# Kernel tuning notes

Measured on AMD Instinct MI355X. Metric: run time of the kernel, lower is better.

The kernel has to match this reference:

```python
import jax, jax.numpy as jnp
import numpy as np
import math

D = 256; H = 8; L = 6; DK = D // H

def _ln(x, g, b):
    m = jnp.mean(x, -1, keepdims=True)
    v = jnp.mean((x - m) ** 2, -1, keepdims=True)
    return (x - m) * jax.lax.rsqrt(v + 1e-5) * g + b

def setup_inputs() -> dict:
    key = jax.random.key(0)
    ks = jax.random.split(key, 16)
    B, N, F, E = 8, 768, 128, 4
    s = 0.02
    inp = {}
    inp['node_feats'] = jax.random.normal(ks[0], (B, N, F), jnp.float32)
    inp['adj'] = jax.random.randint(ks[1], (B, N, N), 0, 2, jnp.int32)
    inp['dist'] = jax.random.uniform(ks[2], (B, N, N), jnp.float32)
    inp['edge_type_oh'] = jax.random.uniform(ks[3], (B, N, N, E), jnp.float32)
    inp['node_proj_w'] = jax.random.normal(ks[4], (F, D), jnp.float32) * s
    inp['node_proj_b'] = jnp.zeros((D,), jnp.float32)
    inp['cls'] = jax.random.normal(ks[5], (1, 1, D), jnp.float32) * s
    inp['etw'] = jax.random.normal(ks[6], (E,), jnp.float32) * s
    inp['noedge_bias'] = jnp.float32(-2.0)
    inp['deg_scale'] = jnp.float32(0.2)
    inp['gamma'] = jnp.float32(0.8)
    inp['v2n'] = jnp.float32(0.1)
    inp['n2v'] = jnp.float32(0.1)
    inp['vself'] = jnp.float32(0.05)
    inp['ln1_g'] = jnp.ones((L, D), jnp.float32); inp['ln1_b'] = jnp.zeros((L, D), jnp.float32)
    inp['qw'] = jax.random.normal(ks[7], (L, D, D), jnp.float32) * s; inp['qb'] = jnp.zeros((L, D), jnp.float32)
    inp['kw'] = jax.random.normal(ks[8], (L, D, D), jnp.float32) * s; inp['kb'] = jnp.zeros((L, D), jnp.float32)
    inp['vw'] = jax.random.normal(ks[9], (L, D, D), jnp.float32) * s; inp['vb'] = jnp.zeros((L, D), jnp.float32)
    inp['ow'] = jax.random.normal(ks[10], (L, D, D), jnp.float32) * s; inp['ob'] = jnp.zeros((L, D), jnp.float32)
    inp['ln2_g'] = jnp.ones((L, D), jnp.float32); inp['ln2_b'] = jnp.zeros((L, D), jnp.float32)
    Dm = int(D * 1.0)  # mlp_ratio=1.0
    inp['fc1w'] = jax.random.normal(ks[11], (L, D, Dm), jnp.float32) * s; inp['fc1b'] = jnp.zeros((L, Dm), jnp.float32)
    inp['fc2w'] = jax.random.normal(ks[12], (L, Dm, D), jnp.float32) * s; inp['fc2b'] = jnp.zeros((L, D), jnp.float32)
    return inp

def _build_bias(adj_f, dist, edge_type_oh, etw, noedge_bias, deg_scale, gamma, v2n, n2v, vself):
    # DynamicAttnBiasBuilder: hard_mask=False, use_degree=True, vnode_spd_mode='replace', gamma != 0
    B, N, _ = adj_f.shape
    T = N + 1
    e = jnp.einsum('bije,e->bij', edge_type_oh, etw) - gamma * dist  # (B,N,N)
    e = jnp.where(adj_f > 0, e, e + noedge_bias)
    deg = adj_f.sum(-1)  # (B,N)
    deg_norm = (deg[:, :, None] + deg[:, None, :]) / (deg.max(axis=1, keepdims=True)[:, :, None] + 1e-6)
    e = e + deg_scale * deg_norm
    bias = jnp.zeros((B, T, T), jnp.float32)
    bias = bias.at[:, 1:, 1:].set(e)
    bias = bias.at[:, 0, 1:].set(v2n)   # vnode_spd_mode == 'replace'
    bias = bias.at[:, 1:, 0].set(n2v)
    bias = bias.at[:, 0, 0].set(vself)
    return bias  # (B,T,T), broadcast over heads

def _mhsa(x, bias, qw, qb, kw, kb, vw, vb, ow, ob):
    B, T, _ = x.shape
    q = (x @ qw + qb).reshape(B, T, H, DK).transpose(0, 2, 1, 3)
    k = (x @ kw + kb).reshape(B, T, H, DK).transpose(0, 2, 1, 3)
    v = (x @ vw + vb).reshape(B, T, H, DK).transpose(0, 2, 1, 3)
    scores = jnp.einsum('bhqd,bhkd->bhqk', q, k) / math.sqrt(DK)
    scores = scores + bias[:, None, :, :]
    attn = jax.nn.softmax(scores, axis=-1)
    out = jnp.einsum('bhqk,bhkd->bhqd', attn, v)
    out = out.transpose(0, 2, 1, 3).reshape(B, T, D)
    return out @ ow + ob

def _forward(node_feats, adj, dist, edge_type_oh, node_proj_w, node_proj_b, cls,
             etw, noedge_bias, deg_scale, gamma, v2n, n2v, vself,
             ln1_g, ln1_b, qw, qb, kw, kb, vw, vb, ow, ob,
             ln2_g, ln2_b, fc1w, fc1b, fc2w, fc2b):
    adj_f = adj.astype(jnp.float32)
    bias = _build_bias(adj_f, dist, edge_type_oh, etw, noedge_bias, deg_scale, gamma, v2n, n2v, vself)
    B = node_feats.shape[0]
    x = node_feats @ node_proj_w + node_proj_b  # (B,N,D)
    x = jnp.concatenate([jnp.broadcast_to(cls, (B, 1, D)), x], axis=1)  # prepend virtual node -> (B,T,D)
    for l in range(L):
        h = _mhsa(_ln(x, ln1_g[l], ln1_b[l]), bias, qw[l], qb[l], kw[l], kb[l], vw[l], vb[l], ow[l], ob[l])
        x = x + h
        m = _ln(x, ln2_g[l], ln2_b[l])
        m = jax.nn.gelu(m @ fc1w[l] + fc1b[l], approximate=False) @ fc2w[l] + fc2b[l]
        x = x + m
    return x

def reference(node_feats, adj, dist, edge_type_oh, node_proj_w, node_proj_b, cls,
              etw, noedge_bias, deg_scale, gamma, v2n, n2v, vself,
              ln1_g, ln1_b, qw, qb, kw, kb, vw, vb, ow, ob,
              ln2_g, ln2_b, fc1w, fc1b, fc2w, fc2b):
    return _forward(node_feats, adj, dist, edge_type_oh, node_proj_w, node_proj_b, cls,
                    etw, noedge_bias, deg_scale, gamma, v2n, n2v, vself,
                    ln1_g, ln1_b, qw, qb, kw, kb, vw, vb, ow, ob,
                    ln2_g, ln2_b, fc1w, fc1b, fc2w, fc2b)
```

## Files before the change

### kernel.cpp

```cpp
#include <hip/hip_runtime.h>
#include <math.h>

#define BB 8
#define NN 768
#define TT 769
#define DD 256
#define HH 8
#define DKK 32
#define FF 128
#define LL 6
#define MM 6152
#define SCALE 0.17677669529663687f
#define TP 832
#define KQP 784
#define KHS (KQP * DKK)
#define GBP 776
#define HP 264
#define WSZ 65536

typedef __attribute__((ext_vector_type(8))) short s16x8;
typedef __attribute__((ext_vector_type(8))) unsigned short u16x8;
typedef __attribute__((ext_vector_type(4))) float f32x4;

__device__ inline short f2bf(float x) {
    unsigned u = __float_as_uint(x);
    unsigned r = (u + 0x7FFFu + ((u >> 16) & 1u)) >> 16;
    return (short)r;
}
__device__ inline float bf2f(unsigned short s) {
    return __uint_as_float(((unsigned)s) << 16);
}
__device__ inline float gelu_f(float x) {
    return 0.5f * x * (1.f + erff(x * 0.70710678118654752f));
}

__global__ __launch_bounds__(256) void deg_kernel(const int* __restrict__ adj,
                                                  float* __restrict__ deg) {
    int row  = blockIdx.x * 4 + (threadIdx.x >> 6);
    int lane = threadIdx.x & 63;
    const int* p = adj + (size_t)row * NN;
    int s = 0;
#pragma unroll
    for (int i = 0; i < NN / 64; ++i) s += p[lane + 64 * i];
#pragma unroll
    for (int off = 32; off > 0; off >>= 1) s += __shfl_xor(s, off);
    if (lane == 0) deg[row] = (float)s;
}

__global__ __launch_bounds__(256) void degmax_kernel(const float* __restrict__ deg,
                                                     float* __restrict__ dmax) {
    __shared__ float red[256];
    int b = blockIdx.x, t = threadIdx.x;
    float m = 0.f;
    for (int i = t; i < NN; i += 256) m = fmaxf(m, deg[b * NN + i]);
    red[t] = m;
    __syncthreads();
    for (int s = 128; s > 0; s >>= 1) {
        if (t < s) red[t] = fmaxf(red[t], red[t + s]);
        __syncthreads();
    }
    if (t == 0) dmax[b] = red[0];
}

__global__ __launch_bounds__(256) void bias_kernel(
    const float* __restrict__ dist, const float* __restrict__ eoh,
    const int* __restrict__ adj, const float* __restrict__ deg,
    const float* __restrict__ dmax, const float* __restrict__ etw,
    const float* __restrict__ noedge, const float* __restrict__ degsc,
    const float* __restrict__ gamma, const float* __restrict__ v2n,
    const float* __restrict__ n2v, const float* __restrict__ vself,
    unsigned short* __restrict__ bias)
{
    long long idx = (long long)blockIdx.x * 256 + threadIdx.x;
    const long long total = (long long)BB * TT * GBP;
    if (idx >= total) return;
    int b  = (int)(idx / ((long long)TT * GBP));
    int r  = (int)(idx % ((long long)TT * GBP));
    int qi = r / GBP, kj = r % GBP;
    float out;
    if (kj >= TT)                out = 0.f;
    else if (qi == 0 && kj == 0) out = vself[0];
    else if (qi == 0)            out = v2n[0];
    else if (kj == 0)            out = n2v[0];
    else {
        int i = qi - 1, j = kj - 1;
        size_t e = ((size_t)b * NN + i) * NN + j;
        float4 oh = *(const float4*)(eoh + 4 * e);
        float val = oh.x * etw[0] + oh.y * etw[1] + oh.z * etw[2] + oh.w * etw[3]
                    - gamma[0] * dist[e];
        if (adj[e] == 0) val += noedge[0];
        val += degsc[0] * (deg[b * NN + i] + deg[b * NN + j]) / (dmax[b] + 1e-6f);
        out = val;
    }
    bias[idx] = (unsigned short)f2bf(out);
}

__global__ __launch_bounds__(256) void nodeproj_ln_kernel(
    const float* __restrict__ nf, const float* __restrict__ w,
    const float* __restrict__ bsv, const float* __restrict__ cls,
    const float* __restrict__ g, const float* __restrict__ bvec,
    float* __restrict__ x, short* __restrict__ xn)
{
    __shared__ float sf[FF];
    __shared__ float red[256];
    int row = blockIdx.x, t = threadIdx.x;
    int b = row / TT, tr = row % TT;
    float y;
    if (tr == 0) {
        y = cls[t];
    } else {
        if (t < FF) sf[t] = nf[((size_t)b * NN + tr - 1) * FF + t];
        __syncthreads();
        y = bsv[t];
#pragma unroll 8
        for (int kk = 0; kk < FF; ++kk) y = fmaf(sf[kk], w[kk * DD + t], y);
    }
    x[(size_t)row * DD + t] = y;
    red[t] = y;
    __syncthreads();
    for (int s = 128; s > 0; s >>= 1) { if (t < s) red[t] += red[t + s]; __syncthreads(); }
    float mean = red[0] * (1.f / DD);
    __syncthreads();
    float d = y - mean;
    red[t] = d * d;
    __syncthreads();
    for (int s = 128; s > 0; s >>= 1) { if (t < s) red[t] += red[t + s]; __syncthreads(); }
    float var = red[0] * (1.f / DD);
    xn[(size_t)row * DD + t] = f2bf(d * rsqrtf(var + 1e-5f) * g[t] + bvec[t]);
}

__global__ __launch_bounds__(256) void wtrans_kernel(
    const float* __restrict__ qw, const float* __restrict__ kw,
    const float* __restrict__ vw, const float* __restrict__ ow,
    const float* __restrict__ f1w, const float* __restrict__ f2w,
    short* __restrict__ wt2)
{
    int mi = blockIdx.x >> 4, kg = blockIdx.x & 15;
    int fam = mi / 6, l = mi % 6;
    const float* W;
    if      (fam == 0) W = qw;
    else if (fam == 1) W = kw;
    else if (fam == 2) W = vw;
    else if (fam == 3) W = ow;
    else if (fam == 4) W = f1w;
    else               W = f2w;
    W += (size_t)l * DD * DD;
    int n = threadIdx.x;
    short* out = wt2 + (size_t)mi * WSZ;
#pragma unroll
    for (int kk = 0; kk < 16; ++kk) {
        int k = kg * 16 + kk;
        float val = W[(size_t)k * DD + n];
        size_t idx = (size_t)(((n >> 4) * 8 + (k >> 5)) * 512
                   + (((k >> 3) & 3) * 16 + (n & 15)) * 8 + (k & 7));
        out[idx] = f2bf(val);
    }
}

__global__ __launch_bounds__(256) void gemm_qkv_kernel(
    const short* __restrict__ A, const short* __restrict__ wtl,
    const float* __restrict__ qb, const float* __restrict__ kb,
    const float* __restrict__ vb,
    short* __restrict__ qh, short* __restrict__ kh, short* __restrict__ vtb)
{
    int t = threadIdx.x;
    int w = t >> 6, lane = t & 63, quad = lane >> 4, m16 = lane & 15;
    int m0 = blockIdx.x * 16;
    int fam = blockIdx.y;
    const short* Wf = wtl + (size_t)fam * 6 * WSZ;
    const float* bsv = fam == 0 ? qb : (fam == 1 ? kb : vb);
    int arow = m0 + m16; if (arow >= MM) arow = MM - 1;
    const short* ap = A + (size_t)arow * DD + quad * 8;
    const short* wbase = Wf + (size_t)(w * 4) * 4096 + lane * 8;
    f32x4 acc[4] = {};
#pragma unroll
    for (int kc = 0; kc < 8; ++kc) {
        s16x8 af = *(const s16x8*)(ap + kc * 32);
#pragma unroll
        for (int nt = 0; nt < 4; ++nt) {
            s16x8 bf = *(const s16x8*)(wbase + (size_t)nt * 4096 + kc * 512);
            acc[nt] = __builtin_amdgcn_mfma_f32_16x16x32_bf16(af, bf, acc[nt], 0, 0, 0);
        }
    }
    if (fam < 2) {
        short* outp = fam == 0 ? qh : kh;
#pragma unroll
        for (int r = 0; r < 4; ++r) {
            int row = m0 + quad * 4 + r;
            if (row < MM) {
                int b = row / TT;
                int tpos = row - b * TT;
                size_t rb = ((size_t)b * HH * KQP + tpos) * DKK;
#pragma unroll
                for (int nt = 0; nt < 4; ++nt) {
                    int col = w * 64 + nt * 16 + m16;
                    float bv = bsv[col];
                    int h = col >> 5, dk = col & 31;
                    outp[rb + (size_t)h * KHS + dk] = f2bf(acc[nt][r] + bv);
                }
            }
        }
    } else {
#pragma unroll
        for (int nt = 0; nt < 4; ++nt) {
            int col = w * 64 + nt * 16 + m16;
            float bv = bsv[col];
            int h = col >> 5, dk = col & 31;
#pragma unroll
            for (int r = 0; r < 4; ++r) {
                int row = m0 + quad * 4 + r;
                if (row < MM) {
                    int b = row / TT;
                    int tpos = row - b * TT;
                    vtb[(((size_t)(b * HH + h)) * DKK + dk) * TP + tpos] =
                        f2bf(acc[nt][r] + bv);
                }
            }
        }
    }
}

__global__ __launch_bounds__(256) void attn_kernel(
    const short* __restrict__ q, const short* __restrict__ k,
    const short* __restrict__ vt, const unsigned short* __restrict__ bias,
    short* __restrict__ o)
{
    __shared__ short Pb[4][16][72];
    int t = threadIdx.x;
    int wid = t >> 6, lane = t & 63;
    int quad = lane >> 4, m16 = lane & 15;
    int bx = blockIdx.x;
    int h4 = bx / 392;
    int rem = bx - h4 * 392;
    int b = rem / 49;
    int qt = rem - b * 49;
    int h = h4 * 4 + wid;
    int q0 = qt * 16;

    size_t rb4[4];
#pragma unroll
    for (int r = 0; r < 4; ++r) {
        int qr = q0 + quad * 4 + r; if (qr >= TT) qr = TT - 1;
        rb4[r] = (size_t)(b * TT + qr) * GBP;
    }

    int qrow = q0 + m16;
    int qc = qrow < TT ? qrow : TT - 1;
    const short* qbase = q + (size_t)(b * HH + h) * KHS;
    s16x8 qa = *(const s16x8*)(qbase + (size_t)qc * DKK + quad * 8);

    const short* kbase = k + (size_t)(b * HH + h) * KHS;
    const short* vbase = vt + (((size_t)(b * HH + h)) * DKK) * TP;

    s16x8 kfA[4], kfB[4], vfA[4], vfB[4];
    unsigned short bbA[16], bbB[16];
    f32x4 sacc[4];
    f32x4 o0 = {0.f, 0.f, 0.f, 0.f};
    f32x4 o1 = {0.f, 0.f, 0.f, 0.f};
    float ls[4] = {0.f, 0.f, 0.f, 0.f};

#define LOADK_(DST, CC)                                                         \
    {                                                                           \
        _Pragma("unroll") for (int s = 0; s < 4; ++s) {                         \
            int kr = (CC) * 64 + s * 16 + m16;                                  \
            int kcl = kr < TT ? kr : TT - 1;                                    \
            DST[s] = *(const s16x8*)(kbase + (size_t)kcl * DKK + quad * 8);     \
        }                                                                       \
    }
#define LOADV_(DST, CC)                                                         \
    {                                                                           \
        int jn = (CC) * 64;                                                     \
        DST[0] = *(const s16x8*)(vbase + (size_t)m16 * TP + jn + quad * 8);     \
        DST[1] = *(const s16x8*)(vbase + (size_t)m16 * TP + jn + 32 + quad * 8);\
        DST[2] = *(const s16x8*)(vbase + (size_t)(16 + m16) * TP + jn + quad * 8);\
        DST[3] = *(const s16x8*)(vbase + (size_t)(16 + m16) * TP + jn + 32 + quad * 8);\
    }
#define LOADB_(DST, CC)                                                         \
    {                                                                           \
        _Pragma("unroll") for (int s = 0; s < 4; ++s) {                         \
            int ko = (CC) * 64 + s * 16 + m16;                                  \
            ko = ko < TT ? ko : 0;                                              \
            _Pragma("unroll") for (int r = 0; r < 4; ++r)                       \
                DST[s * 4 + r] = bias[rb4[r] + ko];                             \
        }                                                                       \
    }
#define STEP_(C, KPRE, KUSE, VUSE, VPRE, BUSE, BPRE, DOPREK, DOPREV, DOPREB, DOQK) \
    {                                                                           \
        if (DOPREK) LOADK_(KPRE, (C) + 2);                                      \
        if (DOPREV) LOADV_(VPRE, (C) + 1);                                      \
        if (DOPREB) LOADB_(BPRE, (C) + 1);                                      \
        int j0 = (C) * 64;                                                      \
        _Pragma("unroll") for (int s = 0; s < 4; ++s) {                         \
            int key = j0 + s * 16 + m16;                                        \
            int kv = key < TT;                                                  \
            _Pragma("unroll") for (int r = 0; r < 4; ++r) {                     \
                float bv = bf2f(BUSE[s * 4 + r]);                               \
                float sval = kv ? fmaf(sacc[s][r], SCALE, bv) : -1e30f;         \
                float p = __expf(sval - 8.0f);                                  \
                ls[r] += p;                                                     \
                Pb[wid][quad * 4 + r][s * 16 + m16] = f2bf(p);                  \
            }                                                                   \
        }                                                                       \
        if (DOQK) {                                                             \
            f32x4 z = {0.f, 0.f, 0.f, 0.f};                                     \
            _Pragma("unroll") for (int s = 0; s < 4; ++s)                       \
                sacc[s] = __builtin_amdgcn_mfma_f32_16x16x32_bf16(qa, KUSE[s], z, 0, 0, 0); \
        }                                                                       \
        s16x8 pa0 = *(const s16x8*)&Pb[wid][m16][quad * 8];                     \
        s16x8 pa1 = *(const s16x8*)&Pb[wid][m16][32 + quad * 8];                \
        o0 = __builtin_amdgcn_mfma_f32_16x16x32_bf16(pa0, VUSE[0], o0, 0, 0, 0);\
        o0 = __builtin_amdgcn_mfma_f32_16x16x32_bf16(pa1, VUSE[1], o0, 0, 0, 0);\
        o1 = __builtin_amdgcn_mfma_f32_16x16x32_bf16(pa0, VUSE[2], o1, 0, 0, 0);\
        o1 = __builtin_amdgcn_mfma_f32_16x16x32_bf16(pa1, VUSE[3], o1, 0, 0, 0);\
    }

    LOADK_(kfA, 0);
    LOADK_(kfB, 1);
    LOADV_(vfA, 0);
    LOADB_(bbA, 0);
    {
        f32x4 z = {0.f, 0.f, 0.f, 0.f};
#pragma unroll
        for (int s = 0; s < 4; ++s)
            sacc[s] = __builtin_amdgcn_mfma_f32_16x16x32_bf16(qa, kfA[s], z, 0, 0, 0);
    }

    for (int cc = 0; cc < 5; ++cc) {
        STEP_(2 * cc,     kfA, kfB, vfA, vfB, bbA, bbB, 1, 1, 1, 1)
        STEP_(2 * cc + 1, kfB, kfA, vfB, vfA, bbB, bbA, 1, 1, 1, 1)
    }
    STEP_(10, kfA, kfB, vfA, vfB, bbA, bbB, 1, 1, 1, 1)
    STEP_(11, kfB, kfA, vfB, vfA, bbB, bbA, 0, 1, 1, 1)
    STEP_(12, kfA, kfB, vfA, vfB, bbA, bbB, 0, 0, 0, 0)

#undef STEP_
#undef LOADB_
#undef LOADV_
#undef LOADK_

#pragma unroll
    for (int r = 0; r < 4; ++r) {
        float l = ls[r];
#pragma unroll
        for (int off = 1; off < 16; off <<= 1) l += __shfl_xor(l, off);
        int qr = q0 + quad * 4 + r;
        if (qr < TT) {
            float inv = 1.f / l;
            short* op = o + ((size_t)(b * TT + qr)) * DD + h * DKK;
            op[m16]      = f2bf(o0[r] * inv);
            op[16 + m16] = f2bf(o1[r] * inv);
        }
    }
}

__global__ __launch_bounds__(256) void gemm_oln2_kernel(
    const short* __restrict__ A, const short* __restrict__ Ws,
    const float* __restrict__ bsv, const float* __restrict__ g2,
    const float* __restrict__ b2, float* __restrict__ x, short* __restrict__ xn)
{
    __shared__ float redS[64], redQ[64];
    int t = threadIdx.x;
    int w = t >> 6, lane = t & 63, quad = lane >> 4, m16 = lane & 15;
    int m0 = blockIdx.x * 16;
    int arow = m0 + m16; if (arow >= MM) arow = MM - 1;
    const short* ap = A + (size_t)arow * DD + quad * 8;
    const short* wbase = Ws + (size_t)(w * 4) * 4096 + lane * 8;
    f32x4 acc[4] = {};
#pragma unroll
    for (int kc = 0; kc < 8; ++kc) {
        s16x8 af = *(const s16x8*)(ap + kc * 32);
#pragma unroll
        for (int nt = 0; nt < 4; ++nt) {
            s16x8 bf = *(const s16x8*)(wbase + (size_t)nt * 4096 + kc * 512);
            acc[nt] = __builtin_amdgcn_mfma_f32_16x16x32_bf16(af, bf, acc[nt], 0, 0, 0);
        }
    }
    float vv[4][4], sr[4], qr2[4];
#pragma unroll
    for (int r = 0; r < 4; ++r) { sr[r] = 0.f; qr2[r] = 0.f; }
#pragma unroll
    for (int nt = 0; nt < 4; ++nt) {
        int col = w * 64 + nt * 16 + m16;
        float bv = bsv[col];
#pragma unroll
        for (int r = 0; r < 4; ++r) {
            int row = m0 + quad * 4 + r; int rc = row < MM ? row : MM - 1;
            float v = acc[nt][r] + bv + x[(size_t)rc * DD + col];
            vv[nt][r] = v; sr[r] += v; qr2[r] += v * v;
        }
    }
#pragma unroll
    for (int r = 0; r < 4; ++r)
#pragma unroll
        for (int off = 1; off < 16; off <<= 1) {
            sr[r]  += __shfl_xor(sr[r], off);
            qr2[r] += __shfl_xor(qr2[r], off);
        }
    if (m16 == 0) {
#pragma unroll
        for (int r = 0; r < 4; ++r) {
            redS[w * 16 + quad * 4 + r] = sr[r];
            redQ[w * 16 + quad * 4 + r] = qr2[r];
        }
    }
    __syncthreads();
#pragma unroll
    for (int r = 0; r < 4; ++r) {
        int rl = quad * 4 + r;
        int row = m0 + rl;
        float fs = redS[rl] + redS[16 + rl] + redS[32 + rl] + redS[48 + rl];
        float fq = redQ[rl] + redQ[16 + rl] + redQ[32 + rl] + redQ[48 + rl];
        float mean = fs * (1.f / DD);
        float var = fq * (1.f / DD) - mean * mean;
        float inv = rsqrtf(var + 1e-5f);
        if (row < MM) {
#pragma unroll
            for (int nt = 0; nt < 4; ++nt) {
                int col = w * 64 + nt * 16 + m16;
                float v = vv[nt][r];
                x[(size_t)row * DD + col] = v;
                xn[(size_t)row * DD + col] = f2bf((v - mean) * inv * g2[col] + b2[col]);
            }
        }
    }
}

__global__ __launch_bounds__(256) void mlp_kernel(
    short* __restrict__ xn, const short* __restrict__ W1s,
    const short* __restrict__ W2s, const float* __restrict__ f1b,
    const float* __restrict__ f2b, float* __restrict__ x,
    const float* __restrict__ g1, const float* __restrict__ b1, int donext)
{
    __shared__ short hbuf[16 * HP];
    __shared__ float redS[64], redQ[64];
    int t = threadIdx.x;
    int w = t >> 6, lane = t & 63, quad = lane >> 4, m16 = lane & 15;
    int m0 = blockIdx.x * 16;
    int arow = m0 + m16; if (arow >= MM) arow = MM - 1;
    const short* ap = xn + (size_t)arow * DD + quad * 8;
    const short* w1base = W1s + (size_t)(w * 4) * 4096 + lane * 8;
    const short* w2base = W2s + (size_t)(w * 4) * 4096 + lane * 8;

    f32x4 acc[4] = {};
#pragma unroll
    for (int kc = 0; kc < 8; ++kc) {
        s16x8 af = *(const s16x8*)(ap + kc * 32);
#pragma unroll
        for (int nt = 0; nt < 4; ++nt) {
            s16x8 bf = *(const s16x8*)(w1base + (size_t)nt * 4096 + kc * 512);
            acc[nt] = __builtin_amdgcn_mfma_f32_16x16x32_bf16(af, bf, acc[nt], 0, 0, 0);
        }
    }
#pragma unroll
    for (int nt = 0; nt < 4; ++nt) {
        int col = w * 64 + nt * 16 + m16;
        float fb = f1b[col];
#pragma unroll
        for (int r = 0; r < 4; ++r)
            hbuf[(quad * 4 + r) * HP + col] = f2bf(gelu_f(acc[nt][r] + fb));
    }
    __syncthreads();

    f32x4 acc2[4] = {};
#pragma unroll
    for (int kc = 0; kc < 8; ++kc) {
        s16x8 af = *(const s16x8*)&hbuf[m16 * HP + kc * 32 + quad * 8];
#pragma unroll
        for (int nt = 0; nt < 4; ++nt) {
            s16x8 bf = *(const s16x8*)(w2base + (size_t)nt * 4096 + kc * 512);
            acc2[nt] = __builtin_amdgcn_mfma_f32_16x16x32_bf16(af, bf, acc2[nt], 0, 0, 0);
        }
    }
    float vv[4][4], sr[4], qr2[4];
#pragma unroll
    for (int r = 0; r < 4; ++r) { sr[r] = 0.f; qr2[r] = 0.f; }
#pragma unroll
    for (int nt = 0; nt < 4; ++nt) {
        int col = w * 64 + nt * 16 + m16;
        float bv = f2b[col];
#pragma unroll
        for (int r = 0; r < 4; ++r) {
            int row = m0 + quad * 4 + r; int rc = row < MM ? row : MM - 1;
            float v = acc2[nt][r] + bv + x[(size_t)rc * DD + col];
            vv[nt][r] = v; sr[r] += v; qr2[r] += v * v;
        }
    }
#pragma unroll
    for (int r = 0; r < 4; ++r)
#pragma unroll
        for (int off = 1; off < 16; off <<= 1) {
            sr[r]  += __shfl_xor(sr[r], off);
            qr2[r] += __shfl_xor(qr2[r], off);
        }
    if (m16 == 0) {
#pragma unroll
        for (int r = 0; r < 4; ++r) {
            redS[w * 16 + quad * 4 + r] = sr[r];
            redQ[w * 16 + quad * 4 + r] = qr2[r];
        }
    }
    __syncthreads();
#pragma unroll
    for (int r = 0; r < 4; ++r) {
        int rl = quad * 4 + r;
        int row = m0 + rl;
        float fs = redS[rl] + redS[16 + rl] + redS[32 + rl] + redS[48 + rl];
        float fq = redQ[rl] + redQ[16 + rl] + redQ[32 + rl] + redQ[48 + rl];
        float mean = fs * (1.f / DD);
        float var = fq * (1.f / DD) - mean * mean;
        float inv = rsqrtf(var + 1e-5f);
        if (row < MM) {
#pragma unroll
            for (int nt = 0; nt < 4; ++nt) {
                int col = w * 64 + nt * 16 + m16;
                float v = vv[nt][r];
                x[(size_t)row * DD + col] = v;
                if (donext)
                    xn[(size_t)row * DD + col] =
                        f2bf((v - mean) * inv * g1[col] + b1[col]);
            }
        }
    }
}

extern "C" void kernel_launch(void* const* d_in, const int* in_sizes, int n_in,
                              void* d_out, int out_size, void* d_ws, size_t ws_size,
                              hipStream_t stream)
{
    const float* node_feats = (const float*)d_in[0];
    const int*   adj        = (const int*)d_in[1];
    const float* dist       = (const float*)d_in[2];
    const float* eoh        = (const float*)d_in[3];
    const float* npw        = (const float*)d_in[4];
    const float* npb        = (const float*)d_in[5];
    const float* cls        = (const float*)d_in[6];
    const float* etw        = (const float*)d_in[7];
    const float* noedge     = (const float*)d_in[8];
    const float* degsc      = (const float*)d_in[9];
    const float* gamma      = (const float*)d_in[10];
    const float* v2n        = (const float*)d_in[11];
    const float* n2v        = (const float*)d_in[12];
    const float* vself      = (const float*)d_in[13];
    const float* ln1g = (const float*)d_in[14];
    const float* ln1b = (const float*)d_in[15];
    const float* qw   = (const float*)d_in[16];
    const float* qb   = (const float*)d_in[17];
    const float* kw   = (const float*)d_in[18];
    const float* kb   = (const float*)d_in[19];
    const float* vw   = (const float*)d_in[20];
    const float* vb   = (const float*)d_in[21];
    const float* ow   = (const float*)d_in[22];
    const float* ob   = (const float*)d_in[23];
    const float* ln2g = (const float*)d_in[24];
    const float* ln2b = (const float*)d_in[25];
    const float* f1w  = (const float*)d_in[26];
    const float* f1b  = (const float*)d_in[27];
    const float* f2w  = (const float*)d_in[28];
    const float* f2b  = (const float*)d_in[29];

    float* x  = (float*)d_out;
    char* ws = (char*)d_ws;
    size_t off = 0;
    unsigned short* bias = (unsigned short*)(ws + off); off += (size_t)BB * TT * GBP * 2;
    float* deg  = (float*)(ws + off); off += (size_t)BB * NN * 4;
    float* dmax = (float*)(ws + off); off += 64;
    short* xn16 = (short*)(ws + off); off += (size_t)MM * DD * 2;
    short* qhb  = (short*)(ws + off); off += (size_t)BB * HH * KQP * DKK * 2;
    short* khb  = (short*)(ws + off); off += (size_t)BB * HH * KQP * DKK * 2;
    short* vtb  = (short*)(ws + off); off += (size_t)BB * HH * DKK * TP * 2;
    short* ab16 = (short*)(ws + off); off += (size_t)MM * DD * 2;
    short* wt2  = (short*)(ws + off); off += (size_t)36 * WSZ * 2;

    deg_kernel<<<(BB * NN) / 4, 256, 0, stream>>>(adj, deg);
    degmax_kernel<<<BB, 256, 0, stream>>>(deg, dmax);

    long long total = (long long)BB * TT * GBP;
    bias_kernel<<<(int)((total + 255) / 256), 256, 0, stream>>>(
        dist, eoh, adj, deg, dmax, etw, noedge, degsc, gamma, v2n, n2v, vself, bias);

    nodeproj_ln_kernel<<<MM, 256, 0, stream>>>(node_feats, npw, npb, cls,
                                               ln1g, ln1b, x, xn16);

    wtrans_kernel<<<576, 256, 0, stream>>>(qw, kw, vw, ow, f1w, f2w, wt2);

    dim3 gqkv(385, 3);
    for (int l = 0; l < LL; ++l) {
        size_t bo = (size_t)l * DD;
        gemm_qkv_kernel<<<gqkv, 256, 0, stream>>>(xn16, wt2 + (size_t)l * WSZ,
                                                  qb + bo, kb + bo, vb + bo,
                                                  qhb, khb, vtb);
        attn_kernel<<<784, 256, 0, stream>>>(qhb, khb, vtb, bias, ab16);
        gemm_oln2_kernel<<<385, 256, 0, stream>>>(ab16, wt2 + (size_t)(3 * 6 + l) * WSZ,
                                                  ob + bo, ln2g + bo, ln2b + bo, x, xn16);
        int donext = (l + 1 < LL) ? 1 : 0;
        size_t bn = (size_t)(l + 1 < LL ? l + 1 : 0) * DD;
        mlp_kernel<<<385, 256, 0, stream>>>(xn16, wt2 + (size_t)(4 * 6 + l) * WSZ,
                                            wt2 + (size_t)(5 * 6 + l) * WSZ,
                                            f1b + bo, f2b + bo, x,
                                            ln1g + bn, ln1b + bn, donext);
    }
}
```

Baseline: 751.2 us.

## Fuse attention, output projection, LN2 and MLP into one per-tile kernel

Attention, the output projection with residual and LN2, and the MLP with residual and next-layer LN1 now run in a single kernel. Each 512-thread block covers one 16-row query tile with all 8 heads, one wave per head. The attention output, normalized activations and MLP hidden state stay in shared memory, which removes the ab16 round trip, the xn16 reload and two kernel launches per layer. The cost is fewer blocks (392 instead of 784), larger blocks with more shared memory, and every block re-reading all three weight matrices, which may reduce occupancy and parallelism in the attention phase.

```diff
diff --git a/kernel.cpp b/kernel.cpp
--- a/kernel.cpp
+++ b/kernel.cpp
@@ -220,21 +220,30 @@
     }
 }
 
-__global__ __launch_bounds__(256) void attn_kernel(
+__global__ __launch_bounds__(512) void mega_kernel(
     const short* __restrict__ q, const short* __restrict__ k,
     const short* __restrict__ vt, const unsigned short* __restrict__ bias,
-    short* __restrict__ o)
+    const short* __restrict__ Wo, const short* __restrict__ W1,
+    const short* __restrict__ W2,
+    const float* __restrict__ ob, const float* __restrict__ g2,
+    const float* __restrict__ b2, const float* __restrict__ f1b,
+    const float* __restrict__ f2b, float* __restrict__ x,
+    short* __restrict__ xn, const float* __restrict__ g1,
+    const float* __restrict__ b1, int donext)
 {
-    __shared__ short Pb[4][16][72];
+    __shared__ short Pb[8][16][72];
+    __shared__ short xa[16][HP];
+    __shared__ short xnl[16][HP];
+    __shared__ short hb[16][HP];
+    __shared__ float redS[16][8], redQ[16][8];
+
     int t = threadIdx.x;
-    int wid = t >> 6, lane = t & 63;
+    int w = t >> 6, lane = t & 63;
     int quad = lane >> 4, m16 = lane & 15;
     int bx = blockIdx.x;
-    int h4 = bx / 392;
-    int rem = bx - h4 * 392;
-    int b = rem / 49;
-    int qt = rem - b * 49;
-    int h = h4 * 4 + wid;
+    int b = bx / 49;
+    int qt = bx - b * 49;
+    int h = w;
     int q0 = qt * 16;
 
     size_t rb4[4];
@@ -298,7 +307,7 @@
                 float sval = kv ? fmaf(sacc[s][r], SCALE, bv) : -1e30f;         \
                 float p = __expf(sval - 8.0f);                                  \
                 ls[r] += p;                                                     \
-                Pb[wid][quad * 4 + r][s * 16 + m16] = f2bf(p);                  \
+                Pb[w][quad * 4 + r][s * 16 + m16] = f2bf(p);                    \
             }                                                                   \
         }                                                                       \
         if (DOQK) {                                                             \
@@ -306,8 +315,8 @@
             _Pragma("unroll") for (int s = 0; s < 4; ++s)                       \
                 sacc[s] = __builtin_amdgcn_mfma_f32_16x16x32_bf16(qa, KUSE[s], z, 0, 0, 0); \
         }                                                                       \
-        s16x8 pa0 = *(const s16x8*)&Pb[wid][m16][quad * 8];                     \
-        s16x8 pa1 = *(const s16x8*)&Pb[wid][m16][32 + quad * 8];                \
+        s16x8 pa0 = *(const s16x8*)&Pb[w][m16][quad * 8];                       \
+        s16x8 pa1 = *(const s16x8*)&Pb[w][m16][32 + quad * 8];                  \
         o0 = __builtin_amdgcn_mfma_f32_16x16x32_bf16(pa0, VUSE[0], o0, 0, 0, 0);\
         o0 = __builtin_amdgcn_mfma_f32_16x16x32_bf16(pa1, VUSE[1], o0, 0, 0, 0);\
         o1 = __builtin_amdgcn_mfma_f32_16x16x32_bf16(pa0, VUSE[2], o1, 0, 0, 0);\
@@ -324,7 +333,6 @@
         for (int s = 0; s < 4; ++s)
             sacc[s] = __builtin_amdgcn_mfma_f32_16x16x32_bf16(qa, kfA[s], z, 0, 0, 0);
     }
-
     for (int cc = 0; cc < 5; ++cc) {
         STEP_(2 * cc,     kfA, kfB, vfA, vfB, bbA, bbB, 1, 1, 1, 1)
         STEP_(2 * cc + 1, kfB, kfA, vfB, vfA, bbB, bbA, 1, 1, 1, 1)
@@ -343,181 +351,150 @@
         float l = ls[r];
 #pragma unroll
         for (int off = 1; off < 16; off <<= 1) l += __shfl_xor(l, off);
-        int qr = q0 + quad * 4 + r;
-        if (qr < TT) {
-            float inv = 1.f / l;
-            short* op = o + ((size_t)(b * TT + qr)) * DD + h * DKK;
-            op[m16]      = f2bf(o0[r] * inv);
-            op[16 + m16] = f2bf(o1[r] * inv);
-        }
-    }
-}
-
-__global__ __launch_bounds__(256) void gemm_oln2_kernel(
-    const short* __restrict__ A, const short* __restrict__ Ws,
-    const float* __restrict__ bsv, const float* __restrict__ g2,
-    const float* __restrict__ b2, float* __restrict__ x, short* __restrict__ xn)
-{
-    __shared__ float redS[64], redQ[64];
-    int t = threadIdx.x;
-    int w = t >> 6, lane = t & 63, quad = lane >> 4, m16 = lane & 15;
-    int m0 = blockIdx.x * 16;
-    int arow = m0 + m16; if (arow >= MM) arow = MM - 1;
-    const short* ap = A + (size_t)arow * DD + quad * 8;
-    const short* wbase = Ws + (size_t)(w * 4) * 4096 + lane * 8;
-    f32x4 acc[4] = {};
+        float inv = 1.f / l;
+        int rl = quad * 4 + r;
+        xa[rl][h * DKK + m16]      = f2bf(o0[r] * inv);
+        xa[rl][h * DKK + 16 + m16] = f2bf(o1[r] * inv);
+    }
+    __syncthreads();
+
+    const short* wob = Wo + (size_t)(w * 2) * 4096 + lane * 8;
+    f32x4 acco[2] = {};
 #pragma unroll
     for (int kc = 0; kc < 8; ++kc) {
-        s16x8 af = *(const s16x8*)(ap + kc * 32);
-#pragma unroll
-        for (int nt = 0; nt < 4; ++nt) {
-            s16x8 bf = *(const s16x8*)(wbase + (size_t)nt * 4096 + kc * 512);
-            acc[nt] = __builtin_amdgcn_mfma_f32_16x16x32_bf16(af, bf, acc[nt], 0, 0, 0);
-        }
-    }
-    float vv[4][4], sr[4], qr2[4];
-#pragma unroll
-    for (int r = 0; r < 4; ++r) { sr[r] = 0.f; qr2[r] = 0.f; }
-#pragma unroll
-    for (int nt = 0; nt < 4; ++nt) {
-        int col = w * 64 + nt * 16 + m16;
-        float bv = bsv[col];
+        s16x8 af = *(const s16x8*)&xa[m16][kc * 32 + quad * 8];
+#pragma unroll
+        for (int ntl = 0; ntl < 2; ++ntl) {
+            s16x8 bf = *(const s16x8*)(wob + (size_t)ntl * 4096 + kc * 512);
+            acco[ntl] = __builtin_amdgcn_mfma_f32_16x16x32_bf16(af, bf, acco[ntl], 0, 0, 0);
+        }
+    }
+    float vv[2][4], sr[4], q2[4];
+#pragma unroll
+    for (int r = 0; r < 4; ++r) { sr[r] = 0.f; q2[r] = 0.f; }
+#pragma unroll
+    for (int ntl = 0; ntl < 2; ++ntl) {
+        int col = w * 32 + ntl * 16 + m16;
+        float bv = ob[col];
 #pragma unroll
         for (int r = 0; r < 4; ++r) {
-            int row = m0 + quad * 4 + r; int rc = row < MM ? row : MM - 1;
-            float v = acc[nt][r] + bv + x[(size_t)rc * DD + col];
-            vv[nt][r] = v; sr[r] += v; qr2[r] += v * v;
+            int row = q0 + quad * 4 + r; if (row >= TT) row = TT - 1;
+            float v = acco[ntl][r] + bv + x[((size_t)(b * TT + row)) * DD + col];
+            vv[ntl][r] = v; sr[r] += v; q2[r] += v * v;
         }
     }
 #pragma unroll
     for (int r = 0; r < 4; ++r)
 #pragma unroll
         for (int off = 1; off < 16; off <<= 1) {
-            sr[r]  += __shfl_xor(sr[r], off);
-            qr2[r] += __shfl_xor(qr2[r], off);
+            sr[r] += __shfl_xor(sr[r], off);
+            q2[r] += __shfl_xor(q2[r], off);
         }
     if (m16 == 0) {
 #pragma unroll
         for (int r = 0; r < 4; ++r) {
-            redS[w * 16 + quad * 4 + r] = sr[r];
-            redQ[w * 16 + quad * 4 + r] = qr2[r];
-        }
-    }
-    __syncthreads();
+            redS[quad * 4 + r][w] = sr[r];
+            redQ[quad * 4 + r][w] = q2[r];
+        }
+    }
+    __syncthreads();
+
 #pragma unroll
     for (int r = 0; r < 4; ++r) {
         int rl = quad * 4 + r;
-        int row = m0 + rl;
-        float fs = redS[rl] + redS[16 + rl] + redS[32 + rl] + redS[48 + rl];
-        float fq = redQ[rl] + redQ[16 + rl] + redQ[32 + rl] + redQ[48 + rl];
+        float fs = 0.f, fq = 0.f;
+#pragma unroll
+        for (int j = 0; j < 8; ++j) { fs += redS[rl][j]; fq += redQ[rl][j]; }
         float mean = fs * (1.f / DD);
         float var = fq * (1.f / DD) - mean * mean;
         float inv = rsqrtf(var + 1e-5f);
-        if (row < MM) {
-#pragma unroll
-            for (int nt = 0; nt < 4; ++nt) {
-                int col = w * 64 + nt * 16 + m16;
-                float v = vv[nt][r];
-                x[(size_t)row * DD + col] = v;
-                xn[(size_t)row * DD + col] = f2bf((v - mean) * inv * g2[col] + b2[col]);
-            }
-        }
-    }
-}
-
-__global__ __launch_bounds__(256) void mlp_kernel(
-    short* __restrict__ xn, const short* __restrict__ W1s,
-    const short* __restrict__ W2s, const float* __restrict__ f1b,
-    const float* __restrict__ f2b, float* __restrict__ x,
-    const float* __restrict__ g1, const float* __restrict__ b1, int donext)
-{
-    __shared__ short hbuf[16 * HP];
-    __shared__ float redS[64], redQ[64];
-    int t = threadIdx.x;
-    int w = t >> 6, lane = t & 63, quad = lane >> 4, m16 = lane & 15;
-    int m0 = blockIdx.x * 16;
-    int arow = m0 + m16; if (arow >= MM) arow = MM - 1;
-    const short* ap = xn + (size_t)arow * DD + quad * 8;
-    const short* w1base = W1s + (size_t)(w * 4) * 4096 + lane * 8;
-    const short* w2base = W2s + (size_t)(w * 4) * 4096 + lane * 8;
-
-    f32x4 acc[4] = {};
+#pragma unroll
+        for (int ntl = 0; ntl < 2; ++ntl) {
+            int col = w * 32 + ntl * 16 + m16;
+            xnl[rl][col] = f2bf((vv[ntl][r] - mean) * inv * g2[col] + b2[col]);
+        }
+    }
+    __syncthreads();
+
+    const short* w1b = W1 + (size_t)(w * 2) * 4096 + lane * 8;
+    f32x4 acc1[2] = {};
 #pragma unroll
     for (int kc = 0; kc < 8; ++kc) {
-        s16x8 af = *(const s16x8*)(ap + kc * 32);
-#pragma unroll
-        for (int nt = 0; nt < 4; ++nt) {
-            s16x8 bf = *(const s16x8*)(w1base + (size_t)nt * 4096 + kc * 512);
-            acc[nt] = __builtin_amdgcn_mfma_f32_16x16x32_bf16(af, bf, acc[nt], 0, 0, 0);
-        }
-    }
-#pragma unroll
-    for (int nt = 0; nt < 4; ++nt) {
-        int col = w * 64 + nt * 16 + m16;
+        s16x8 af = *(const s16x8*)&xnl[m16][kc * 32 + quad * 8];
+#pragma unroll
+        for (int ntl = 0; ntl < 2; ++ntl) {
+            s16x8 bf = *(const s16x8*)(w1b + (size_t)ntl * 4096 + kc * 512);
+            acc1[ntl] = __builtin_amdgcn_mfma_f32_16x16x32_bf16(af, bf, acc1[ntl], 0, 0, 0);
+        }
+    }
+#pragma unroll
+    for (int ntl = 0; ntl < 2; ++ntl) {
+        int col = w * 32 + ntl * 16 + m16;
         float fb = f1b[col];
 #pragma unroll
         for (int r = 0; r < 4; ++r)
-            hbuf[(quad * 4 + r) * HP + col] = f2bf(gelu_f(acc[nt][r] + fb));
-    }
-    __syncthreads();
-
-    f32x4 acc2[4] = {};
+            hb[quad * 4 + r][col] = f2bf(gelu_f(acc1[ntl][r] + fb));
+    }
+    __syncthreads();
+
+    const short* w2b = W2 + (size_t)(w * 2) * 4096 + lane * 8;
+    f32x4 acc2[2] = {};
 #pragma unroll
     for (int kc = 0; kc < 8; ++kc) {
-        s16x8 af = *(const s16x8*)&hbuf[m16 * HP + kc * 32 + quad * 8];
-#pragma unroll
-        for (int nt = 0; nt < 4; ++nt) {
-            s16x8 bf = *(const s16x8*)(w2base + (size_t)nt * 4096 + kc * 512);
-            acc2[nt] = __builtin_amdgcn_mfma_f32_16x16x32_bf16(af, bf, acc2[nt], 0, 0, 0);
-        }
-    }
-    float vv[4][4], sr[4], qr2[4];
-#pragma unroll
-    for (int r = 0; r < 4; ++r) { sr[r] = 0.f; qr2[r] = 0.f; }
-#pragma unroll
-    for (int nt = 0; nt < 4; ++nt) {
-        int col = w * 64 + nt * 16 + m16;
+        s16x8 af = *(const s16x8*)&hb[m16][kc * 32 + quad * 8];
+#pragma unroll
+        for (int ntl = 0; ntl < 2; ++ntl) {
+            s16x8 bf = *(const s16x8*)(w2b + (size_t)ntl * 4096 + kc * 512);
+            acc2[ntl] = __builtin_amdgcn_mfma_f32_16x16x32_bf16(af, bf, acc2[ntl], 0, 0, 0);
+        }
+    }
+#pragma unroll
+    for (int r = 0; r < 4; ++r) { sr[r] = 0.f; q2[r] = 0.f; }
+#pragma unroll
+    for (int ntl = 0; ntl < 2; ++ntl) {
+        int col = w * 32 + ntl * 16 + m16;
         float bv = f2b[col];
 #pragma unroll
         for (int r = 0; r < 4; ++r) {
-            int row = m0 + quad * 4 + r; int rc = row < MM ? row : MM - 1;
-            float v = acc2[nt][r] + bv + x[(size_t)rc * DD + col];
-            vv[nt][r] = v; sr[r] += v; qr2[r] += v * v;
+            float v = acc2[ntl][r] + bv + vv[ntl][r];
+            vv[ntl][r] = v; sr[r] += v; q2[r] += v * v;
         }
     }
 #pragma unroll
     for (int r = 0; r < 4; ++r)
 #pragma unroll
         for (int off = 1; off < 16; off <<= 1) {
-            sr[r]  += __shfl_xor(sr[r], off);
-            qr2[r] += __shfl_xor(qr2[r], off);
+            sr[r] += __shfl_xor(sr[r], off);
+            q2[r] += __shfl_xor(q2[r], off);
         }
     if (m16 == 0) {
 #pragma unroll
         for (int r = 0; r < 4; ++r) {
-            redS[w * 16 + quad * 4 + r] = sr[r];
-            redQ[w * 16 + quad * 4 + r] = qr2[r];
-        }
-    }
-    __syncthreads();
+            redS[quad * 4 + r][w] = sr[r];
+            redQ[quad * 4 + r][w] = q2[r];
+        }
+    }
+    __syncthreads();
+
 #pragma unroll
     for (int r = 0; r < 4; ++r) {
         int rl = quad * 4 + r;
-        int row = m0 + rl;
-        float fs = redS[rl] + redS[16 + rl] + redS[32 + rl] + redS[48 + rl];
-        float fq = redQ[rl] + redQ[16 + rl] + redQ[32 + rl] + redQ[48 + rl];
+        int row = q0 + rl;
+        float fs = 0.f, fq = 0.f;
+#pragma unroll
+        for (int j = 0; j < 8; ++j) { fs += redS[rl][j]; fq += redQ[rl][j]; }
         float mean = fs * (1.f / DD);
         float var = fq * (1.f / DD) - mean * mean;
         float inv = rsqrtf(var + 1e-5f);
-        if (row < MM) {
-#pragma unroll
-            for (int nt = 0; nt < 4; ++nt) {
-                int col = w * 64 + nt * 16 + m16;
-                float v = vv[nt][r];
-                x[(size_t)row * DD + col] = v;
+        if (row < TT) {
+            size_t grow = (size_t)(b * TT + row) * DD;
+#pragma unroll
+            for (int ntl = 0; ntl < 2; ++ntl) {
+                int col = w * 32 + ntl * 16 + m16;
+                float v = vv[ntl][r];
+                x[grow + col] = v;
                 if (donext)
-                    xn[(size_t)row * DD + col] =
-                        f2bf((v - mean) * inv * g1[col] + b1[col]);
+                    xn[grow + col] = f2bf((v - mean) * inv * g1[col] + b1[col]);
             }
         }
     }
@@ -568,7 +545,6 @@
     short* qhb  = (short*)(ws + off); off += (size_t)BB * HH * KQP * DKK * 2;
     short* khb  = (short*)(ws + off); off += (size_t)BB * HH * KQP * DKK * 2;
     short* vtb  = (short*)(ws + off); off += (size_t)BB * HH * DKK * TP * 2;
-    short* ab16 = (short*)(ws + off); off += (size_t)MM * DD * 2;
     short* wt2  = (short*)(ws + off); off += (size_t)36 * WSZ * 2;
 
     deg_kernel<<<(BB * NN) / 4, 256, 0, stream>>>(adj, deg);
@@ -589,14 +565,14 @@
         gemm_qkv_kernel<<<gqkv, 256, 0, stream>>>(xn16, wt2 + (size_t)l * WSZ,
                                                   qb + bo, kb + bo, vb + bo,
                                                   qhb, khb, vtb);
-        attn_kernel<<<784, 256, 0, stream>>>(qhb, khb, vtb, bias, ab16);
-        gemm_oln2_kernel<<<385, 256, 0, stream>>>(ab16, wt2 + (size_t)(3 * 6 + l) * WSZ,
-                                                  ob + bo, ln2g + bo, ln2b + bo, x, xn16);
         int donext = (l + 1 < LL) ? 1 : 0;
         size_t bn = (size_t)(l + 1 < LL ? l + 1 : 0) * DD;
-        mlp_kernel<<<385, 256, 0, stream>>>(xn16, wt2 + (size_t)(4 * 6 + l) * WSZ,
-                                            wt2 + (size_t)(5 * 6 + l) * WSZ,
-                                            f1b + bo, f2b + bo, x,
-                                            ln1g + bn, ln1b + bn, donext);
-    }
-}
+        mega_kernel<<<392, 512, 0, stream>>>(
+            qhb, khb, vtb, bias,
+            wt2 + (size_t)(3 * 6 + l) * WSZ,
+            wt2 + (size_t)(4 * 6 + l) * WSZ,
+            wt2 + (size_t)(5 * 6 + l) * WSZ,
+            ob + bo, ln2g + bo, ln2b + bo, f1b + bo, f2b + bo,
+            x, xn16, ln1g + bn, ln1b + bn, donext);
+    }
+}
```

Result: faster. 730.7 us (-2.7%).
